# Kernel optimization log

Measured on AMD Instinct MI355X. Metric: run time of the kernel, lower is better.

## Reference

```python
import jax, jax.numpy as jnp
import numpy as np

N_QUBITS = 4
LAYERS = 1

# state has shape [N] + [2]*n; qubit w lives on axis w+1 (wire 0 = most significant, as in PennyLane)

def _apply_ry(state, theta, w, n):
    s0 = jnp.take(state, 0, axis=w + 1)
    s1 = jnp.take(state, 1, axis=w + 1)
    shp = (-1,) + (1,) * (n - 1)
    c = jnp.cos(theta / 2).reshape(shp)
    s = jnp.sin(theta / 2).reshape(shp)
    return jnp.stack([c * s0 - s * s1, s * s0 + c * s1], axis=w + 1)


def _apply_crx(state, theta, ctrl, tgt, n):
    sub0 = jnp.take(state, 0, axis=ctrl + 1)  # control = 0 subspace (unchanged)
    sub1 = jnp.take(state, 1, axis=ctrl + 1)  # control = 1 subspace -> RX on target
    t_ax = tgt + 1 if tgt < ctrl else tgt     # target axis inside sub1 ([N] at axis 0)
    a0 = jnp.take(sub1, 0, axis=t_ax)
    a1 = jnp.take(sub1, 1, axis=t_ax)
    shp = (-1,) + (1,) * (n - 2)
    c = jnp.cos(theta / 2).reshape(shp).astype(state.dtype)
    s = jnp.sin(theta / 2).reshape(shp).astype(state.dtype)
    new1 = jnp.stack([c * a0 - 1j * s * a1, -1j * s * a0 + c * a1], axis=t_ax)
    return jnp.stack([sub0, new1], axis=ctrl + 1)


def run_circuit(params):
    """Ansatz 14 (arXiv:1905.10876) applied to |0...0>, batched over tokens. params: [N, 4*n*layers]."""
    n = N_QUBITS
    N = params.shape[0]
    state = jnp.zeros((N,) + (2,) * n, jnp.complex64)
    state = state.at[(slice(None),) + (0,) * n].set(1.0)
    idx = 0
    for _ in range(LAYERS):
        for i in range(n):
            state = _apply_ry(state, params[:, idx], i, n); idx += 1
        for i in range(n - 1, -1, -1):
            state = _apply_crx(state, params[:, idx], i, (i + 1) % n, n); idx += 1
        for i in range(n):
            state = _apply_ry(state, params[:, idx], i, n); idx += 1
        for i in [n - 1] + list(range(n - 1)):
            state = _apply_crx(state, params[:, idx], i, (i - 1) % n, n); idx += 1
    return state


def measure_xyz(state, n):
    """<X_w>, <Y_w>, <Z_w> for all wires; order matches the PennyLane qnode (all X, all Y, all Z)."""
    N = state.shape[0]
    xs, ys, zs = [], [], []
    for w in range(n):
        s0 = jnp.take(state, 0, axis=w + 1).reshape(N, -1)
        s1 = jnp.take(state, 1, axis=w + 1).reshape(N, -1)
        prod = jnp.sum(jnp.conj(s0) * s1, axis=-1)
        xs.append(2.0 * jnp.real(prod))
        ys.append(2.0 * jnp.imag(prod))
        zs.append(jnp.sum(jnp.abs(s0) ** 2 - jnp.abs(s1) ** 2, axis=-1))
    return jnp.stack(xs + ys + zs, axis=-1)  # [N, 3n]


def setup_inputs() -> dict:
    key = jax.random.key(0)
    k = jax.random.split(key, 7)
    B, L, S, H, E = 2, 2048, 2048, 8, 64
    n_params = 4 * N_QUBITS * LAYERS  # 16
    queries = jax.random.normal(k[0], (B, L, H, E), jnp.float32)
    keys = jax.random.normal(k[1], (B, S, H, E), jnp.float32)
    values = jax.random.normal(k[2], (B, S, H, E), jnp.float32)
    W_angles = jax.random.normal(k[3], (n_params, E), jnp.float32) * 0.125   # Linear(d_model -> 16)
    b_angles = jax.random.normal(k[4], (n_params,), jnp.float32) * 0.125
    W_out = jax.random.normal(k[5], (E, 3 * N_QUBITS), jnp.float32) * 0.28   # Linear(12 -> d_model)
    b_out = jax.random.normal(k[6], (E,), jnp.float32) * 0.28
    return {"queries": queries, "keys": keys, "values": values,
            "W_angles": W_angles, "b_angles": b_angles, "W_out": W_out, "b_out": b_out}


def reference(queries, keys, values, W_angles, b_angles, W_out, b_out):
    B, L, H, E = queries.shape
    S = keys.shape[1]
    scale = 1.0 / np.sqrt(E)
    # quantum encoding of values: angles -> PQC from |0> -> X/Y/Z expvals -> linear map to d_model
    angles = jnp.einsum('bshd,pd->bshp', values, W_angles) + b_angles      # [B,S,H,16]
    state = run_circuit(angles.reshape(-1, angles.shape[-1]))              # [N, 2,2,2,2]
    meas = measure_xyz(state, N_QUBITS)                                    # [N, 12]
    qev = (meas @ W_out.T + b_out).reshape(B, S, H, E)                     # [B,S,H,D]
    # classical attention (eval mode: dropout = identity)
    scores = jnp.einsum('blhe,bshe->bhls', queries, keys)
    mask = jnp.triu(jnp.ones((L, S), bool), 1)
    scores = jnp.where(mask[None, None], -1e9, scores)
    A = jax.nn.softmax(scale * scores, axis=-1)
    return jnp.einsum('bhls,bshd->blhd', A, qev)
```

## Files before the change

kernel.cpp:

```cpp
#include <hip/hip_runtime.h>

#define NP   16
#define EDIM 64
#define HH   8
#define BB   2
#define LL   2048
#define SS   2048
#define TQ   64
#define TS   64
#define NQT  (LL / TQ)
#define NPAIR (NQT / 2)
#define LDP  72

typedef __attribute__((ext_vector_type(8))) short bf16x8;
typedef __attribute__((ext_vector_type(4))) float f32x4;

__device__ __forceinline__ unsigned short f2bf(float f) {
    union { float ff; unsigned int i; } x; x.ff = f;
    unsigned int r = x.i + 0x7fffu + ((x.i >> 16) & 1u);
    return (unsigned short)(r >> 16);
}
__device__ __forceinline__ unsigned int pk2(float a, float b) {
    return (unsigned int)f2bf(a) | ((unsigned int)f2bf(b) << 16);
}

__device__ __forceinline__ void stage16s(const float* __restrict__ g, unsigned short* l, float sc) {
    const float4* gp = (const float4*)g;
    float4 v0 = gp[0], v1 = gp[1], v2 = gp[2], v3 = gp[3];
    v0.x *= sc; v0.y *= sc; v0.z *= sc; v0.w *= sc;
    v1.x *= sc; v1.y *= sc; v1.z *= sc; v1.w *= sc;
    v2.x *= sc; v2.y *= sc; v2.z *= sc; v2.w *= sc;
    v3.x *= sc; v3.y *= sc; v3.z *= sc; v3.w *= sc;
    uint4 w0, w1;
    w0.x = pk2(v0.x, v0.y); w0.y = pk2(v0.z, v0.w);
    w0.z = pk2(v1.x, v1.y); w0.w = pk2(v1.z, v1.w);
    w1.x = pk2(v2.x, v2.y); w1.y = pk2(v2.z, v2.w);
    w1.z = pk2(v3.x, v3.y); w1.w = pk2(v3.z, v3.w);
    ((uint4*)l)[0] = w0; ((uint4*)l)[1] = w1;
}

#define INV4PI 0.07957747154594767f

__global__ __launch_bounds__(64)
void qevT_kernel(const float* __restrict__ values,
                 const float* __restrict__ key,
                 const float* __restrict__ Wang,
                 const float* __restrict__ bang,
                 const float* __restrict__ Wout,
                 const float* __restrict__ bout,
                 unsigned short* __restrict__ qevb,
                 unsigned short* __restrict__ Kb)
{
    __shared__ float Lv[64 * 68];
    __shared__ float sW[NP * EDIM];
    __shared__ float sWo[EDIM * 12];
    __shared__ float sba[NP];
    __shared__ float sbo[EDIM];

    const int tid = threadIdx.x;
    const int s0  = blockIdx.x * 64;
    const int h   = blockIdx.y;
    const int b   = blockIdx.z;

    for (int i = tid; i < NP * EDIM; i += 64) sW[i]  = Wang[i];
    for (int i = tid; i < EDIM * 12; i += 64) sWo[i] = Wout[i];
    if (tid < NP) sba[tid] = bang[tid];
    sbo[tid] = bout[tid];

    const float* vb = values + ((size_t)b * SS * HH + h) * EDIM;
#pragma unroll
    for (int i = 0; i < 16; i++) {
        const int row = (tid >> 2) + 16 * (i & 3);
        const int c4  = (tid & 3) + 4 * (i >> 2);
        float4 v = *(const float4*)(vb + (size_t)(s0 + row) * HH * EDIM + c4 * 4);
        *(float4*)&Lv[row * 68 + c4 * 4] = v;
    }
    __syncthreads();

    float ang[NP];
#pragma unroll
    for (int p = 0; p < NP; p++) ang[p] = sba[p];
#pragma unroll
    for (int c = 0; c < 16; c++) {
        float4 vv = *(const float4*)&Lv[tid * 68 + c * 4];
#pragma unroll
        for (int p = 0; p < NP; p++) {
            float a = ang[p];
            a = fmaf(sW[p * EDIM + c * 4 + 0], vv.x, a);
            a = fmaf(sW[p * EDIM + c * 4 + 1], vv.y, a);
            a = fmaf(sW[p * EDIM + c * 4 + 2], vv.z, a);
            a = fmaf(sW[p * EDIM + c * 4 + 3], vv.w, a);
            ang[p] = a;
        }
    }

    float sr[16], si[16];
#pragma unroll
    for (int i = 0; i < 16; i++) { sr[i] = 0.f; si[i] = 0.f; }
    sr[0] = 1.f;

    auto RY = [&](int w, float th) {
        float s = __builtin_amdgcn_sinf(th * INV4PI);
        float c = __builtin_amdgcn_cosf(th * INV4PI);
        const int bit = 8 >> w;
#pragma unroll
        for (int i = 0; i < 16; i++) {
            if (!(i & bit)) {
                const int j = i | bit;
                float a0r = sr[i], a0i = si[i], a1r = sr[j], a1i = si[j];
                sr[i] = c * a0r - s * a1r;  si[i] = c * a0i - s * a1i;
                sr[j] = s * a0r + c * a1r;  si[j] = s * a0i + c * a1i;
            }
        }
    };
    auto CRX = [&](int cw, int tw, float th) {
        float s = __builtin_amdgcn_sinf(th * INV4PI);
        float c = __builtin_amdgcn_cosf(th * INV4PI);
        const int cbit = 8 >> cw, tbit = 8 >> tw;
#pragma unroll
        for (int i = 0; i < 16; i++) {
            if ((i & cbit) && !(i & tbit)) {
                const int j = i | tbit;
                float a0r = sr[i], a0i = si[i], a1r = sr[j], a1i = si[j];
                sr[i] =  c * a0r + s * a1i;  si[i] =  c * a0i - s * a1r;
                sr[j] =  s * a0i + c * a1r;  si[j] = -s * a0r + c * a1i;
            }
        }
    };

    RY(0, ang[0]); RY(1, ang[1]); RY(2, ang[2]); RY(3, ang[3]);
    CRX(3, 0, ang[4]); CRX(2, 3, ang[5]); CRX(1, 2, ang[6]); CRX(0, 1, ang[7]);
    RY(0, ang[8]); RY(1, ang[9]); RY(2, ang[10]); RY(3, ang[11]);
    CRX(3, 2, ang[12]); CRX(0, 3, ang[13]); CRX(1, 0, ang[14]); CRX(2, 1, ang[15]);

    float meas[12];
#pragma unroll
    for (int w = 0; w < 4; w++) {
        const int bit = 8 >> w;
        float pr = 0.f, pi = 0.f, z = 0.f;
#pragma unroll
        for (int i = 0; i < 16; i++) {
            if (!(i & bit)) {
                const int j = i | bit;
                pr += sr[i] * sr[j] + si[i] * si[j];
                pi += sr[i] * si[j] - si[i] * sr[j];
                z  += sr[i] * sr[i] + si[i] * si[i] - sr[j] * sr[j] - si[j] * si[j];
            }
        }
        meas[w] = 2.f * pr; meas[4 + w] = 2.f * pi; meas[8 + w] = z;
    }

    unsigned short* ob = qevb + ((size_t)(b * HH + h) * EDIM) * SS + s0 + tid;
#pragma unroll
    for (int e = 0; e < EDIM; e++) {
        float o = sbo[e];
#pragma unroll
        for (int mm = 0; mm < 12; mm++) o = fmaf(meas[mm], sWo[e * 12 + mm], o);
        ob[(size_t)e * SS] = f2bf(o);
    }

    const float* ks = key + ((size_t)b * SS * HH + h) * EDIM;
    unsigned short* kd = Kb + ((size_t)(b * HH + h) * SS + s0) * EDIM;
#pragma unroll
    for (int i = 0; i < 16; i++) {
        const int row = (tid >> 2) + 16 * (i & 3);
        const int c4  = (tid & 3) + 4 * (i >> 2);
        float4 v = *(const float4*)(ks + (size_t)(s0 + row) * HH * EDIM + c4 * 4);
        uint2 w2; w2.x = pk2(v.x, v.y); w2.y = pk2(v.z, v.w);
        *(uint2*)&kd[row * EDIM + c4 * 4] = w2;
    }
}

__global__ __launch_bounds__(256)
void attn4_kernel(const float* __restrict__ qry,
                  const unsigned short* __restrict__ Kb,
                  const unsigned short* __restrict__ Vb,
                  float* __restrict__ out)
{
    __shared__ unsigned short Qs[TQ * LDP];
    __shared__ unsigned short Ks[TS * LDP];
    __shared__ unsigned short Vt[EDIM * LDP];
    __shared__ unsigned short Ps[TQ * LDP];

    const int tid  = threadIdx.x;
    const int bx   = blockIdx.x;
    const int h    = blockIdx.y;
    const int b    = blockIdx.z;
    const int w    = tid >> 6;
    const int lane = tid & 63;
    const int ml   = lane & 15;
    const int quad = lane >> 4;
    const int srow = tid >> 2;
    const int sch  = tid & 3;

    const unsigned short* kbase = Kb + (size_t)(b * HH + h) * SS * EDIM;
    const unsigned short* vbase = Vb + (size_t)(b * HH + h) * EDIM * SS;
    const unsigned short* kgl = kbase + (size_t)srow * EDIM + sch * 16;
    const unsigned short* vgl = vbase + (size_t)srow * SS  + sch * 16;
    unsigned short* ksl = &Ks[srow * LDP + sch * 16];
    unsigned short* vsl = &Vt[srow * LDP + sch * 16];

    const short onev = (ml == 0) ? (short)0x3F80 : (short)0;
    bf16x8 onesf = { onev, onev, onev, onev, onev, onev, onev, onev };

    for (int pass = 0; pass < 2; ++pass) {
        const int qt = pass ? (NQT - 1 - bx) : bx;
        const int q0 = qt * TQ;

        stage16s(qry + (((size_t)b * LL + q0 + srow) * HH + h) * EDIM + sch * 16,
                 &Qs[srow * LDP + sch * 16], 0.125f);

        uint4 kr0 = ((const uint4*)kgl)[0];
        uint4 kr1 = ((const uint4*)kgl)[1];
        uint4 vr0 = ((const uint4*)vgl)[0];
        uint4 vr1 = ((const uint4*)vgl)[1];

        f32x4 oacc[4];
        f32x4 lacc = (f32x4)(0.f);
#pragma unroll
        for (int i = 0; i < 4; i++) oacc[i] = (f32x4)(0.f);
        bf16x8 a0, a1;

        for (int t = 0; t <= qt; ++t) {
            __syncthreads();
            *(uint4*)ksl = kr0; *(uint4*)(ksl + 8) = kr1;
            *(uint4*)vsl = vr0; *(uint4*)(vsl + 8) = vr1;
            __syncthreads();

            if (t == 0) {
                a0 = *(const bf16x8*)&Qs[(16 * w + ml) * LDP + quad * 8];
                a1 = *(const bf16x8*)&Qs[(16 * w + ml) * LDP + quad * 8 + 32];
            }
            if (t < qt) {
                const unsigned short* kp = kgl + (size_t)(t + 1) * TS * EDIM;
                const unsigned short* vp = vgl + (t + 1) * TS;
                kr0 = ((const uint4*)kp)[0]; kr1 = ((const uint4*)kp)[1];
                vr0 = ((const uint4*)vp)[0]; vr1 = ((const uint4*)vp)[1];
            }

            f32x4 sac[4];
#pragma unroll
            for (int nt = 0; nt < 4; nt++) {
                bf16x8 b0 = *(const bf16x8*)&Ks[(16 * nt + ml) * LDP + quad * 8];
                bf16x8 b1 = *(const bf16x8*)&Ks[(16 * nt + ml) * LDP + quad * 8 + 32];
                sac[nt] = __builtin_amdgcn_mfma_f32_16x16x32_bf16(a0, b0, (f32x4)(0.f), 0, 0, 0);
                sac[nt] = __builtin_amdgcn_mfma_f32_16x16x32_bf16(a1, b1, sac[nt], 0, 0, 0);
            }

            const bool diag = (t == qt);
#pragma unroll
            for (int nt = 0; nt < 4; nt++)
#pragma unroll
                for (int r = 0; r < 4; r++) {
                    float p = __expf(sac[nt][r]);
                    if (diag && (16 * nt + ml > 16 * w + 4 * quad + r)) p = 0.f;
                    Ps[(16 * w + 4 * quad + r) * LDP + 16 * nt + ml] = f2bf(p);
                }

            bf16x8 p0 = *(const bf16x8*)&Ps[(16 * w + ml) * LDP + quad * 8];
            bf16x8 p1 = *(const bf16x8*)&Ps[(16 * w + ml) * LDP + quad * 8 + 32];
#pragma unroll
            for (int nt = 0; nt < 4; nt++) {
                bf16x8 v0 = *(const bf16x8*)&Vt[(16 * nt + ml) * LDP + quad * 8];
                bf16x8 v1 = *(const bf16x8*)&Vt[(16 * nt + ml) * LDP + quad * 8 + 32];
                oacc[nt] = __builtin_amdgcn_mfma_f32_16x16x32_bf16(p0, v0, oacc[nt], 0, 0, 0);
                oacc[nt] = __builtin_amdgcn_mfma_f32_16x16x32_bf16(p1, v1, oacc[nt], 0, 0, 0);
            }
            lacc = __builtin_amdgcn_mfma_f32_16x16x32_bf16(p0, onesf, lacc, 0, 0, 0);
            lacc = __builtin_amdgcn_mfma_f32_16x16x32_bf16(p1, onesf, lacc, 0, 0, 0);
        }

        float inv[4];
#pragma unroll
        for (int r = 0; r < 4; r++) {
            float ls = __shfl(lacc[r], lane & 48, 64);
            inv[r] = 1.f / ls;
        }
#pragma unroll
        for (int nt = 0; nt < 4; nt++)
#pragma unroll
            for (int r = 0; r < 4; r++) {
                const int row = q0 + 16 * w + 4 * quad + r;
                out[(((size_t)b * LL + row) * HH + h) * EDIM + 16 * nt + ml] = oacc[nt][r] * inv[r];
            }
    }
}

extern "C" void kernel_launch(void* const* d_in, const int* in_sizes, int n_in,
                              void* d_out, int out_size, void* d_ws, size_t ws_size,
                              hipStream_t stream)
{
    const float* qry  = (const float*)d_in[0];
    const float* key  = (const float*)d_in[1];
    const float* val  = (const float*)d_in[2];
    const float* Wang = (const float*)d_in[3];
    const float* bang = (const float*)d_in[4];
    const float* Wout = (const float*)d_in[5];
    const float* bout = (const float*)d_in[6];
    float* out = (float*)d_out;

    unsigned short* qevb = (unsigned short*)d_ws;
    unsigned short* Kb   = (unsigned short*)((char*)d_ws + (size_t)BB * HH * EDIM * SS * 2);

    (void)in_sizes; (void)n_in; (void)out_size; (void)ws_size;

    qevT_kernel<<<dim3(SS / 64, HH, BB), 64, 0, stream>>>(val, key, Wang, bang, Wout, bout, qevb, Kb);
    attn4_kernel<<<dim3(NPAIR, HH, BB), 256, 0, stream>>>(qry, Kb, qevb, out);
}
```

Baseline: 123.0 us.

## Load K/V fragments directly from global memory and restructure qev precompute

The attention kernel stops staging K and V tiles through shared memory with barriers and software prefetch. Each wave now reads its MFMA operand fragments straight from global memory (L2/cache), which removes two barriers per tile at the cost of redundant global reads across the four waves. The qev kernel drops the values LDS staging and reads per-thread rows directly, precomputes all sin/cos values up front, blocks the output projection by 16, and changes the key conversion to coalesced indexing. P is now converted to bf16 by truncation instead of rounding, which is cheaper but slightly less accurate.

```diff
diff --git a/kernel.cpp b/kernel.cpp
--- a/kernel.cpp
+++ b/kernel.cpp
@@ -20,6 +20,10 @@
     unsigned int r = x.i + 0x7fffu + ((x.i >> 16) & 1u);
     return (unsigned short)(r >> 16);
 }
+__device__ __forceinline__ unsigned short truncbf(float f) {
+    union { float ff; unsigned int i; } x; x.ff = f;
+    return (unsigned short)(x.i >> 16);
+}
 __device__ __forceinline__ unsigned int pk2(float a, float b) {
     return (unsigned int)f2bf(a) | ((unsigned int)f2bf(b) << 16);
 }
@@ -27,22 +31,18 @@
 __device__ __forceinline__ void stage16s(const float* __restrict__ g, unsigned short* l, float sc) {
     const float4* gp = (const float4*)g;
     float4 v0 = gp[0], v1 = gp[1], v2 = gp[2], v3 = gp[3];
-    v0.x *= sc; v0.y *= sc; v0.z *= sc; v0.w *= sc;
-    v1.x *= sc; v1.y *= sc; v1.z *= sc; v1.w *= sc;
-    v2.x *= sc; v2.y *= sc; v2.z *= sc; v2.w *= sc;
-    v3.x *= sc; v3.y *= sc; v3.z *= sc; v3.w *= sc;
     uint4 w0, w1;
-    w0.x = pk2(v0.x, v0.y); w0.y = pk2(v0.z, v0.w);
-    w0.z = pk2(v1.x, v1.y); w0.w = pk2(v1.z, v1.w);
-    w1.x = pk2(v2.x, v2.y); w1.y = pk2(v2.z, v2.w);
-    w1.z = pk2(v3.x, v3.y); w1.w = pk2(v3.z, v3.w);
+    w0.x = pk2(v0.x * sc, v0.y * sc); w0.y = pk2(v0.z * sc, v0.w * sc);
+    w0.z = pk2(v1.x * sc, v1.y * sc); w0.w = pk2(v1.z * sc, v1.w * sc);
+    w1.x = pk2(v2.x * sc, v2.y * sc); w1.y = pk2(v2.z * sc, v2.w * sc);
+    w1.z = pk2(v3.x * sc, v3.y * sc); w1.w = pk2(v3.z * sc, v3.w * sc);
     ((uint4*)l)[0] = w0; ((uint4*)l)[1] = w1;
 }
 
 #define INV4PI 0.07957747154594767f
 
 __global__ __launch_bounds__(64)
-void qevT_kernel(const float* __restrict__ values,
+void qev2_kernel(const float* __restrict__ values,
                  const float* __restrict__ key,
                  const float* __restrict__ Wang,
                  const float* __restrict__ bang,
@@ -51,7 +51,6 @@
                  unsigned short* __restrict__ qevb,
                  unsigned short* __restrict__ Kb)
 {
-    __shared__ float Lv[64 * 68];
     __shared__ float sW[NP * EDIM];
     __shared__ float sWo[EDIM * 12];
     __shared__ float sba[NP];
@@ -62,27 +61,21 @@
     const int h   = blockIdx.y;
     const int b   = blockIdx.z;
 
-    for (int i = tid; i < NP * EDIM; i += 64) sW[i]  = Wang[i];
-    for (int i = tid; i < EDIM * 12; i += 64) sWo[i] = Wout[i];
+#pragma unroll
+    for (int i = 0; i < 4; i++) ((float4*)sW)[i * 64 + tid] = ((const float4*)Wang)[i * 64 + tid];
+#pragma unroll
+    for (int i = 0; i < 3; i++) ((float4*)sWo)[i * 64 + tid] = ((const float4*)Wout)[i * 64 + tid];
     if (tid < NP) sba[tid] = bang[tid];
     sbo[tid] = bout[tid];
-
-    const float* vb = values + ((size_t)b * SS * HH + h) * EDIM;
-#pragma unroll
-    for (int i = 0; i < 16; i++) {
-        const int row = (tid >> 2) + 16 * (i & 3);
-        const int c4  = (tid & 3) + 4 * (i >> 2);
-        float4 v = *(const float4*)(vb + (size_t)(s0 + row) * HH * EDIM + c4 * 4);
-        *(float4*)&Lv[row * 68 + c4 * 4] = v;
-    }
     __syncthreads();
 
+    const float* vptr = values + ((size_t)(b * SS + s0 + tid) * HH + h) * EDIM;
     float ang[NP];
 #pragma unroll
     for (int p = 0; p < NP; p++) ang[p] = sba[p];
 #pragma unroll
     for (int c = 0; c < 16; c++) {
-        float4 vv = *(const float4*)&Lv[tid * 68 + c * 4];
+        float4 vv = ((const float4*)vptr)[c];
 #pragma unroll
         for (int p = 0; p < NP; p++) {
             float a = ang[p];
@@ -94,14 +87,20 @@
         }
     }
 
+    float sc[NP], cc[NP];
+#pragma unroll
+    for (int p = 0; p < NP; p++) {
+        float u = ang[p] * INV4PI;
+        sc[p] = __builtin_amdgcn_sinf(u);
+        cc[p] = __builtin_amdgcn_cosf(u);
+    }
+
     float sr[16], si[16];
 #pragma unroll
     for (int i = 0; i < 16; i++) { sr[i] = 0.f; si[i] = 0.f; }
     sr[0] = 1.f;
 
-    auto RY = [&](int w, float th) {
-        float s = __builtin_amdgcn_sinf(th * INV4PI);
-        float c = __builtin_amdgcn_cosf(th * INV4PI);
+    auto RY = [&](int w, float s, float c) {
         const int bit = 8 >> w;
 #pragma unroll
         for (int i = 0; i < 16; i++) {
@@ -113,9 +112,7 @@
             }
         }
     };
-    auto CRX = [&](int cw, int tw, float th) {
-        float s = __builtin_amdgcn_sinf(th * INV4PI);
-        float c = __builtin_amdgcn_cosf(th * INV4PI);
+    auto CRX = [&](int cw, int tw, float s, float c) {
         const int cbit = 8 >> cw, tbit = 8 >> tw;
 #pragma unroll
         for (int i = 0; i < 16; i++) {
@@ -128,10 +125,10 @@
         }
     };
 
-    RY(0, ang[0]); RY(1, ang[1]); RY(2, ang[2]); RY(3, ang[3]);
-    CRX(3, 0, ang[4]); CRX(2, 3, ang[5]); CRX(1, 2, ang[6]); CRX(0, 1, ang[7]);
-    RY(0, ang[8]); RY(1, ang[9]); RY(2, ang[10]); RY(3, ang[11]);
-    CRX(3, 2, ang[12]); CRX(0, 3, ang[13]); CRX(1, 0, ang[14]); CRX(2, 1, ang[15]);
+    RY(0, sc[0], cc[0]); RY(1, sc[1], cc[1]); RY(2, sc[2], cc[2]); RY(3, sc[3], cc[3]);
+    CRX(3, 0, sc[4], cc[4]); CRX(2, 3, sc[5], cc[5]); CRX(1, 2, sc[6], cc[6]); CRX(0, 1, sc[7], cc[7]);
+    RY(0, sc[8], cc[8]); RY(1, sc[9], cc[9]); RY(2, sc[10], cc[10]); RY(3, sc[11], cc[11]);
+    CRX(3, 2, sc[12], cc[12]); CRX(0, 3, sc[13], cc[13]); CRX(1, 0, sc[14], cc[14]); CRX(2, 1, sc[15], cc[15]);
 
     float meas[12];
 #pragma unroll
@@ -152,34 +149,40 @@
 
     unsigned short* ob = qevb + ((size_t)(b * HH + h) * EDIM) * SS + s0 + tid;
 #pragma unroll
-    for (int e = 0; e < EDIM; e++) {
-        float o = sbo[e];
-#pragma unroll
-        for (int mm = 0; mm < 12; mm++) o = fmaf(meas[mm], sWo[e * 12 + mm], o);
-        ob[(size_t)e * SS] = f2bf(o);
+    for (int eb = 0; eb < 4; eb++) {
+        float acc[16];
+#pragma unroll
+        for (int j = 0; j < 16; j++) acc[j] = sbo[eb * 16 + j];
+#pragma unroll
+        for (int mm = 0; mm < 12; mm++)
+#pragma unroll
+            for (int j = 0; j < 16; j++)
+                acc[j] = fmaf(meas[mm], sWo[(eb * 16 + j) * 12 + mm], acc[j]);
+#pragma unroll
+        for (int j = 0; j < 16; j++)
+            ob[(size_t)(eb * 16 + j) * SS] = f2bf(acc[j]);
     }
 
     const float* ks = key + ((size_t)b * SS * HH + h) * EDIM;
     unsigned short* kd = Kb + ((size_t)(b * HH + h) * SS + s0) * EDIM;
 #pragma unroll
     for (int i = 0; i < 16; i++) {
-        const int row = (tid >> 2) + 16 * (i & 3);
-        const int c4  = (tid & 3) + 4 * (i >> 2);
-        float4 v = *(const float4*)(ks + (size_t)(s0 + row) * HH * EDIM + c4 * 4);
+        const int u   = i * 64 + tid;
+        const int row = u >> 4;
+        const int ch  = u & 15;
+        float4 v = *(const float4*)(ks + (size_t)(s0 + row) * HH * EDIM + ch * 4);
         uint2 w2; w2.x = pk2(v.x, v.y); w2.y = pk2(v.z, v.w);
-        *(uint2*)&kd[row * EDIM + c4 * 4] = w2;
+        *(uint2*)&kd[row * EDIM + ch * 4] = w2;
     }
 }
 
 __global__ __launch_bounds__(256)
-void attn4_kernel(const float* __restrict__ qry,
+void attn5_kernel(const float* __restrict__ qry,
                   const unsigned short* __restrict__ Kb,
                   const unsigned short* __restrict__ Vb,
                   float* __restrict__ out)
 {
     __shared__ unsigned short Qs[TQ * LDP];
-    __shared__ unsigned short Ks[TS * LDP];
-    __shared__ unsigned short Vt[EDIM * LDP];
     __shared__ unsigned short Ps[TQ * LDP];
 
     const int tid  = threadIdx.x;
@@ -195,10 +198,6 @@
 
     const unsigned short* kbase = Kb + (size_t)(b * HH + h) * SS * EDIM;
     const unsigned short* vbase = Vb + (size_t)(b * HH + h) * EDIM * SS;
-    const unsigned short* kgl = kbase + (size_t)srow * EDIM + sch * 16;
-    const unsigned short* vgl = vbase + (size_t)srow * SS  + sch * 16;
-    unsigned short* ksl = &Ks[srow * LDP + sch * 16];
-    unsigned short* vsl = &Vt[srow * LDP + sch * 16];
 
     const short onev = (ml == 0) ? (short)0x3F80 : (short)0;
     bf16x8 onesf = { onev, onev, onev, onev, onev, onev, onev, onev };
@@ -207,42 +206,28 @@
         const int qt = pass ? (NQT - 1 - bx) : bx;
         const int q0 = qt * TQ;
 
+        __syncthreads();
         stage16s(qry + (((size_t)b * LL + q0 + srow) * HH + h) * EDIM + sch * 16,
                  &Qs[srow * LDP + sch * 16], 0.125f);
-
-        uint4 kr0 = ((const uint4*)kgl)[0];
-        uint4 kr1 = ((const uint4*)kgl)[1];
-        uint4 vr0 = ((const uint4*)vgl)[0];
-        uint4 vr1 = ((const uint4*)vgl)[1];
+        __syncthreads();
+
+        bf16x8 a0 = *(const bf16x8*)&Qs[(16 * w + ml) * LDP + quad * 8];
+        bf16x8 a1 = *(const bf16x8*)&Qs[(16 * w + ml) * LDP + quad * 8 + 32];
 
         f32x4 oacc[4];
         f32x4 lacc = (f32x4)(0.f);
 #pragma unroll
         for (int i = 0; i < 4; i++) oacc[i] = (f32x4)(0.f);
-        bf16x8 a0, a1;
 
         for (int t = 0; t <= qt; ++t) {
-            __syncthreads();
-            *(uint4*)ksl = kr0; *(uint4*)(ksl + 8) = kr1;
-            *(uint4*)vsl = vr0; *(uint4*)(vsl + 8) = vr1;
-            __syncthreads();
-
-            if (t == 0) {
-                a0 = *(const bf16x8*)&Qs[(16 * w + ml) * LDP + quad * 8];
-                a1 = *(const bf16x8*)&Qs[(16 * w + ml) * LDP + quad * 8 + 32];
-            }
-            if (t < qt) {
-                const unsigned short* kp = kgl + (size_t)(t + 1) * TS * EDIM;
-                const unsigned short* vp = vgl + (t + 1) * TS;
-                kr0 = ((const uint4*)kp)[0]; kr1 = ((const uint4*)kp)[1];
-                vr0 = ((const uint4*)vp)[0]; vr1 = ((const uint4*)vp)[1];
-            }
-
+            const int s0e = t * TS;
+
+            const unsigned short* kr = kbase + (size_t)(s0e + ml) * EDIM + quad * 8;
             f32x4 sac[4];
 #pragma unroll
             for (int nt = 0; nt < 4; nt++) {
-                bf16x8 b0 = *(const bf16x8*)&Ks[(16 * nt + ml) * LDP + quad * 8];
-                bf16x8 b1 = *(const bf16x8*)&Ks[(16 * nt + ml) * LDP + quad * 8 + 32];
+                bf16x8 b0 = *(const bf16x8*)(kr + nt * 16 * EDIM);
+                bf16x8 b1 = *(const bf16x8*)(kr + nt * 16 * EDIM + 32);
                 sac[nt] = __builtin_amdgcn_mfma_f32_16x16x32_bf16(a0, b0, (f32x4)(0.f), 0, 0, 0);
                 sac[nt] = __builtin_amdgcn_mfma_f32_16x16x32_bf16(a1, b1, sac[nt], 0, 0, 0);
             }
@@ -254,15 +239,17 @@
                 for (int r = 0; r < 4; r++) {
                     float p = __expf(sac[nt][r]);
                     if (diag && (16 * nt + ml > 16 * w + 4 * quad + r)) p = 0.f;
-                    Ps[(16 * w + 4 * quad + r) * LDP + 16 * nt + ml] = f2bf(p);
+                    Ps[(16 * w + 4 * quad + r) * LDP + 16 * nt + ml] = truncbf(p);
                 }
 
             bf16x8 p0 = *(const bf16x8*)&Ps[(16 * w + ml) * LDP + quad * 8];
             bf16x8 p1 = *(const bf16x8*)&Ps[(16 * w + ml) * LDP + quad * 8 + 32];
+
+            const unsigned short* vr = vbase + (size_t)ml * SS + s0e + quad * 8;
 #pragma unroll
             for (int nt = 0; nt < 4; nt++) {
-                bf16x8 v0 = *(const bf16x8*)&Vt[(16 * nt + ml) * LDP + quad * 8];
-                bf16x8 v1 = *(const bf16x8*)&Vt[(16 * nt + ml) * LDP + quad * 8 + 32];
+                bf16x8 v0 = *(const bf16x8*)(vr + (size_t)(nt * 16) * SS);
+                bf16x8 v1 = *(const bf16x8*)(vr + (size_t)(nt * 16) * SS + 32);
                 oacc[nt] = __builtin_amdgcn_mfma_f32_16x16x32_bf16(p0, v0, oacc[nt], 0, 0, 0);
                 oacc[nt] = __builtin_amdgcn_mfma_f32_16x16x32_bf16(p1, v1, oacc[nt], 0, 0, 0);
             }
@@ -304,6 +291,6 @@
 
     (void)in_sizes; (void)n_in; (void)out_size; (void)ws_size;
 
-    qevT_kernel<<<dim3(SS / 64, HH, BB), 64, 0, stream>>>(val, key, Wang, bang, Wout, bout, qevb, Kb);
-    attn4_kernel<<<dim3(NPAIR, HH, BB), 256, 0, stream>>>(qry, Kb, qevb, out);
-}
+    qev2_kernel<<<dim3(SS / 64, HH, BB), 64, 0, stream>>>(val, key, Wang, bang, Wout, bout, qevb, Kb);
+    attn5_kernel<<<dim3(NPAIR, HH, BB), 256, 0, stream>>>(qry, Kb, qevb, out);
+}
```

Result: slower. 154.0 us (+25.2%).
